# Optimization experiments

Hardware: AMD Instinct MI355X
Metric: run time of the kernel (lower is better)

## Reference

```python
import jax, jax.numpy as jnp
import numpy as np

B, T, L, H = 128, 256, 2, 512  # batch, seq_len, num_layers, hidden_size


def setup_inputs() -> dict:
    key = jax.random.key(0)
    k0, k1, k2, k3, k4 = jax.random.split(key, 5)
    s = 1.0 / np.sqrt(H).astype(np.float32)  # PyTorch LSTMCell init scale
    H0 = jax.random.normal(k0, (B, T, H), jnp.float32)
    # layers[l][k] for l in range(L), k in {0: depth cell, 1: time cell}
    Wih = jax.random.uniform(k1, (L, 2, 4 * H, H), jnp.float32, -s, s)
    Whh = jax.random.uniform(k2, (L, 2, 4 * H, H), jnp.float32, -s, s)
    bih = jax.random.uniform(k3, (L, 2, 4 * H), jnp.float32, -s, s)
    bhh = jax.random.uniform(k4, (L, 2, 4 * H), jnp.float32, -s, s)
    return {"H0": H0, "Wih": Wih, "Whh": Whh, "bih": bih, "bhh": bhh}


def _lstm_cell(x, h, c, wih, whh, b):
    # PyTorch LSTMCell gate order: i, f, g, o
    gates = x @ wih.T + h @ whh.T + b  # (B, 4H)
    i, f, g, o = jnp.split(gates, 4, axis=-1)
    c_new = jax.nn.sigmoid(f) * c + jax.nn.sigmoid(i) * jnp.tanh(g)
    h_new = jax.nn.sigmoid(o) * jnp.tanh(c_new)
    return h_new, c_new


def _forward(H0, Wih, Whh, bih, bhh):
    b = bih + bhh  # fuse the two bias terms

    def step(carry, h0_t):
        H1, M1 = carry  # (B, L, H) time-recurrent states
        h0 = h0_t  # (B, H) input at this timestep
        m0 = jnp.zeros_like(h0)  # M0 is all-zeros in the original when mem=None
        h1s, m1s = [], []
        for l in range(L):  # small static layer loop
            h1, m1 = H1[:, l], M1[:, l]
            h0, m0 = _lstm_cell(h1, h0, m0, Wih[l, 0], Whh[l, 0], b[l, 0])
            h1, m1 = _lstm_cell(h0, h1, m1, Wih[l, 1], Whh[l, 1], b[l, 1])
            h1s.append(h1)
            m1s.append(m1)
        return (jnp.stack(h1s, 1), jnp.stack(m1s, 1)), (h0, m0)

    zeros_LH = jnp.zeros((H0.shape[0], L, H), H0.dtype)
    (H1f, M1f), (H0_seq, M0_seq) = jax.lax.scan(
        step, (zeros_LH, zeros_LH), jnp.swapaxes(H0, 0, 1)
    )
    H0_out = jnp.swapaxes(H0_seq, 0, 1)  # (B, T, H)
    M0_out = jnp.swapaxes(M0_seq, 0, 1)  # (B, T, H)
    # batch_first=True -> no transpose of H1/M1 (stay (B, L, H))
    return H0_out, H1f, M0_out, M1f


def reference(H0, Wih, Whh, bih, bhh):
    # Matches torch return (H0, (H1, M0, M1)), flattened to a tuple of arrays.
    return _forward(H0, Wih, Whh, bih, bhh)
```

## Files before the change

### kernel.cpp

```cpp
#include <hip/hip_runtime.h>
#include <math.h>


static constexpr int Hn = 512;
static constexpr int Bn = 128;
static constexpr int Tn = 256;
static constexpr long THn = (long)Tn * Hn;
static constexpr long LBH = (long)Bn * Hn;
static constexpr int NBLK = 256;
static constexpr int NROUND = 2 * Tn + 1;

typedef __attribute__((ext_vector_type(8))) short short8;
typedef __attribute__((ext_vector_type(4))) float floatx4;

__device__ __forceinline__ unsigned short f2bf(float f) {
    unsigned u = __builtin_bit_cast(unsigned, f);
    unsigned r = u + 0x7FFFu + ((u >> 16) & 1u);
    return (unsigned short)(r >> 16);
}
__device__ __forceinline__ unsigned pk2(float a, float b) {
    return (unsigned)f2bf(a) | ((unsigned)f2bf(b) << 16);
}
__device__ __forceinline__ float sel4(float a, float b, float cc, float d, int s) {
    float r = a;
    r = (s == 1) ? b : r;
    r = (s == 2) ? cc : r;
    r = (s == 3) ? d : r;
    return r;
}
__device__ __forceinline__ float selc(floatx4 v, int s) {
    float r = v[0];
    r = (s == 1) ? v[1] : r;
    r = (s == 2) ? v[2] : r;
    r = (s == 3) ? v[3] : r;
    return r;
}

__device__ __forceinline__ void st16_sc(unsigned short* p, unsigned short v) {
    asm volatile("global_store_short %0, %1, off sc1" :: "v"(p), "v"(v) : "memory");
}
__device__ __forceinline__ void st32_sc(float* p, float v) {
    asm volatile("global_store_dword %0, %1, off sc1" :: "v"(p), "v"(v) : "memory");
}

struct Params {
    const float* H0in;
    const float* Wih; const float* Whh;
    const float* bih; const float* bhh;
    unsigned short* h0A; unsigned short* h0B;
    unsigned short* H1b;
    float* m0;
    float* outH0; float* outH1; float* outM0; float* outM1;
    unsigned* bar;
};

struct RoundDesc {
    const unsigned short* x;
    const unsigned short* hB;
    const float* hF;
    const float* cin;
    unsigned short* hOutB;
    float* coutA;
    long cAs;
    float* hOut2; long h2s;
    float* cOut2; long c2s;
};

__device__ __forceinline__ void gridBarrier(unsigned* bar, int leafIdx, unsigned r) {
    asm volatile("s_waitcnt vmcnt(0)" ::: "memory");
    __syncthreads();
    if (threadIdx.x == 0) {
        unsigned prev = __hip_atomic_fetch_add(&bar[leafIdx * 16], 1u,
                                               __ATOMIC_RELAXED, __HIP_MEMORY_SCOPE_AGENT);
        if ((prev & 31u) == 31u) {
            __hip_atomic_fetch_add(&bar[128], 1u, __ATOMIC_RELAXED, __HIP_MEMORY_SCOPE_AGENT);
        }
        const unsigned target = 8u * (r + 1u);
        while (__hip_atomic_load(&bar[128], __ATOMIC_RELAXED, __HIP_MEMORY_SCOPE_AGENT) < target) {
            __builtin_amdgcn_s_sleep(2);
        }
    }
    __syncthreads();
    if (threadIdx.x < 64) {
        asm volatile("buffer_inv sc1" ::: "memory");
        asm volatile("s_waitcnt vmcnt(0)" ::: "memory");
    }
    __syncthreads();
    asm volatile("" ::: "memory");
}

__device__ __forceinline__ void loadChunk(char* dst, const float* Wih, const float* Whh,
                                          int cell, int jt, int tid) {
    const int rw = tid >> 3;
    const int jj = rw >> 2, g = rw & 3;
    const long nrow = (long)cell * 2048 + (long)g * 512 + jt * 8 + jj;
    const float* baseI = Wih + nrow * 512;
    const float* baseH = Whh + nrow * 512;
    const int k0 = (tid & 7) * 128;
    #pragma unroll
    for (int i = 0; i < 16; ++i) {
        int k = k0 + i * 8;
        const float* src = (k < 512) ? (baseI + k) : (baseH + (k - 512));
        float4 v0 = *(const float4*)src;
        float4 v1 = *(const float4*)(src + 4);
        uint4 w = {pk2(v0.x, v0.y), pk2(v0.z, v0.w), pk2(v1.x, v1.y), pk2(v1.z, v1.w)};
        int byteOff = (k >> 5) * 2048 + rw * 64 + ((k >> 3) & 3) * 16;
        *(uint4*)(dst + byteOff) = w;
    }
}

template<int KIND>
__device__ __forceinline__ void runCell(const RoundDesc& D, const char* chunk,
                                        const float bias[2][4], int jt, int row0,
                                        int c, int q, float cst[2]) {
    const long arow = row0 + c;
    const int g = c & 3;
    const int cu = c >> 2;

    short8 afr[32];
    #pragma unroll
    for (int ks = 0; ks < 16; ++ks)
        afr[ks] = *(const short8*)(D.x + arow * 512 + ks * 32 + q * 8);
    if constexpr (KIND == 0) {
        #pragma unroll
        for (int ks = 0; ks < 16; ++ks) {
            const float* hp = D.hF + arow * THn + ks * 32 + q * 8;
            float4 v0 = *(const float4*)(hp);
            float4 v1 = *(const float4*)(hp + 4);
            uint4 w = {pk2(v0.x, v0.y), pk2(v0.z, v0.w),
                       pk2(v1.x, v1.y), pk2(v1.z, v1.w)};
            afr[16 + ks] = __builtin_bit_cast(short8, w);
        }
    } else {
        #pragma unroll
        for (int ks = 0; ks < 16; ++ks)
            afr[16 + ks] = *(const short8*)(D.hB + arow * 512 + ks * 32 + q * 8);
    }
    float cin0 = 0.f, cin1 = 0.f;
    if constexpr (KIND == 2) {
        const int row = row0 + q * 4 + g;
        cin0 = D.cin[(long)row * 512 + jt * 8 + cu];
        cin1 = D.cin[(long)row * 512 + jt * 8 + 4 + cu];
    }

    floatx4 acc0 = {0.f, 0.f, 0.f, 0.f};
    floatx4 acc1 = {0.f, 0.f, 0.f, 0.f};
    const char* base = chunk + (c * 64 + q * 16);
    #pragma unroll
    for (int ks = 0; ks < 32; ++ks) {
        short8 b0 = *(const short8*)(base + ks * 2048);
        short8 b1 = *(const short8*)(base + ks * 2048 + 1024);
        acc0 = __builtin_amdgcn_mfma_f32_16x16x32_bf16(afr[ks], b0, acc0, 0, 0, 0);
        acc1 = __builtin_amdgcn_mfma_f32_16x16x32_bf16(afr[ks], b1, acc1, 0, 0, 0);
    }

    #pragma unroll
    for (int nf = 0; nf < 2; ++nf) {
        floatx4 acc = nf ? acc1 : acc0;
        float s0 = selc(acc, g);
        float s1 = __shfl_xor(selc(acc, g ^ 1), 1);
        float s2 = __shfl_xor(selc(acc, g ^ 2), 2);
        float s3 = __shfl_xor(selc(acc, g ^ 3), 3);
        float iv = sel4(s0, s1, s2, s3, g)     + bias[nf][0];
        float fv = sel4(s0, s1, s2, s3, g ^ 1) + bias[nf][1];
        float gv = sel4(s0, s1, s2, s3, g ^ 2) + bias[nf][2];
        float ov = sel4(s0, s1, s2, s3, g ^ 3) + bias[nf][3];

        const int row = row0 + q * 4 + g;
        const int jglob = jt * 8 + nf * 4 + cu;
        float cold;
        if constexpr (KIND == 0)      cold = 0.f;
        else if constexpr (KIND == 2) cold = nf ? cin1 : cin0;
        else                          cold = cst[nf];
        float si = 1.f / (1.f + expf(-iv));
        float sf = 1.f / (1.f + expf(-fv));
        float so = 1.f / (1.f + expf(-ov));
        float cn = sf * cold + si * tanhf(gv);
        float hn = so * tanhf(cn);

        st16_sc(D.hOutB + (long)row * 512 + jglob, f2bf(hn));
        if constexpr (KIND == 0 || KIND == 2) {
            st32_sc(D.coutA + (long)row * D.cAs + jglob, cn);
        }
        if constexpr (KIND == 2) {
            st32_sc(D.hOut2 + (long)row * THn + jglob, hn);
        }
        if constexpr (KIND == 1 || KIND == 3) {
            cst[nf] = cn;
            if (D.hOut2) {
                st32_sc(D.hOut2 + (long)row * 1024 + jglob, hn);
                st32_sc(D.cOut2 + (long)row * 1024 + jglob, cn);
            }
        }
    }
}

__global__ __launch_bounds__(256, 1) void grid_lstm_persist(Params P) {
    __shared__ char smem[2 * 65536];

    const int tid = threadIdx.x;
    const int lane = tid & 63;
    const int wid = tid >> 6;
    const int c = lane & 15;
    const int q = lane >> 4;
    const int blk = blockIdx.x;
    const int pair = blk >> 1;
    const int half = blk & 1;
    const int jt = pair & 63;
    const bool hiPair = pair >= 64;
    const int cellA = hiPair ? 3 : 0;
    const int cellB = hiPair ? 2 : 1;
    const int leafIdx = blk & 7;

    loadChunk(smem,         P.Wih, P.Whh, cellA, jt, tid);
    loadChunk(smem + 65536, P.Wih, P.Whh, cellB, jt, tid);

    float biasA[2][4], biasB[2][4];
    {
        const int cuu = c >> 2;
        #pragma unroll
        for (int nf = 0; nf < 2; ++nf) {
            int j = jt * 8 + nf * 4 + cuu;
            #pragma unroll
            for (int g2 = 0; g2 < 4; ++g2) {
                long ia = (long)cellA * 2048 + (long)g2 * 512 + j;
                long ib = (long)cellB * 2048 + (long)g2 * 512 + j;
                biasA[nf][g2] = P.bih[ia] + P.bhh[ia];
                biasB[nf][g2] = P.bih[ib] + P.bhh[ib];
            }
        }
    }
    __syncthreads();

    const int row0 = half * 64 + wid * 16;
    float cst[2] = {0.f, 0.f};
    float cstDummy[2] = {0.f, 0.f};

    for (int r = 0; r < NROUND; ++r) {
        const int t = r >> 1;
        const bool stB = (r & 1) != 0;

        if (!stB) {
            if (!hiPair) {
                if (t < Tn) {
                    int p = t & 1;
                    RoundDesc D{};
                    D.x = P.H1b + ((long)p * 2 + 0) * LBH;
                    D.hF = P.H0in + (long)t * Hn;
                    D.hOutB = P.h0A;
                    D.coutA = P.m0; D.cAs = 512;
                    runCell<0>(D, smem, biasA, jt, row0, c, q, cstDummy);
                }
            } else {
                int tc = t - 1;
                if (tc >= 0) {
                    int p = tc & 1;
                    RoundDesc D{};
                    D.x = P.h0B;
                    D.hB = P.H1b + ((long)p * 2 + 1) * LBH;
                    D.hOutB = P.H1b + ((long)(1 - p) * 2 + 1) * LBH;
                    if (tc == Tn - 1) {
                        D.hOut2 = P.outH1 + Hn;
                        D.cOut2 = P.outM1 + Hn;
                    }
                    runCell<3>(D, smem, biasA, jt, row0, c, q, cst);
                }
            }
        } else {
            int p = t & 1;
            if (!hiPair) {
                RoundDesc D{};
                D.x = P.h0A;
                D.hB = P.H1b + ((long)p * 2 + 0) * LBH;
                D.hOutB = P.H1b + ((long)(1 - p) * 2 + 0) * LBH;
                if (t == Tn - 1) {
                    D.hOut2 = P.outH1;
                    D.cOut2 = P.outM1;
                }
                runCell<1>(D, smem + 65536, biasB, jt, row0, c, q, cst);
            } else {
                RoundDesc D{};
                D.x = P.H1b + ((long)p * 2 + 1) * LBH;
                D.hB = P.h0A;
                D.cin = P.m0;
                D.hOutB = P.h0B;
                D.coutA = P.outM0 + (long)t * Hn; D.cAs = THn;
                D.hOut2 = P.outH0 + (long)t * Hn;
                runCell<2>(D, smem + 65536, biasB, jt, row0, c, q, cstDummy);
            }
        }
        if (r + 1 < NROUND) gridBarrier(P.bar, leafIdx, (unsigned)r);
    }
}

extern "C" void kernel_launch(void* const* d_in, const int* in_sizes, int n_in,
                              void* d_out, int out_size, void* d_ws, size_t ws_size,
                              hipStream_t stream) {
    (void)in_sizes; (void)n_in; (void)out_size; (void)ws_size;
    const float* H0in = (const float*)d_in[0];
    const float* Wih  = (const float*)d_in[1];
    const float* Whh  = (const float*)d_in[2];
    const float* bih  = (const float*)d_in[3];
    const float* bhh  = (const float*)d_in[4];
    float* out = (float*)d_out;

    unsigned short* h0A = (unsigned short*)d_ws;
    unsigned short* h0B = h0A + LBH;
    unsigned short* H1b = h0B + LBH;
    float* m0 = (float*)(H1b + 4 * LBH);
    unsigned* bar = (unsigned*)(m0 + LBH);

    size_t zeroBytes = (size_t)((char*)(bar + 256) - (char*)d_ws);
    hipMemsetAsync(d_ws, 0, zeroBytes, stream);

    Params P;
    P.H0in = H0in; P.Wih = Wih; P.Whh = Whh; P.bih = bih; P.bhh = bhh;
    P.h0A = h0A; P.h0B = h0B; P.H1b = H1b; P.m0 = m0;
    P.outH0 = out;
    P.outH1 = out + (long)Bn * THn;
    P.outM0 = P.outH1 + 2 * LBH;
    P.outM1 = P.outM0 + (long)Bn * THn;
    P.bar = bar;

    void* args[] = {&P};
    hipLaunchCooperativeKernel((void*)grid_lstm_persist, dim3(NBLK), dim3(256),
                               args, 0, stream);
}
```

Measured before the change: 5.653 ms.

## Double waves per block, prefetch recurrent operands before barrier, pre-convert input to bf16

Each block now runs 512 threads, with waves split across row groups and column groups, so each wave computes one 16x16 output tile and accumulates over a 32-step K loop instead of two. The recurrent-state fragments for the next round are loaded before the grid barrier, so that load latency overlaps the barrier wait. The fp32 input sequence is converted to bf16 one timestep ahead into a double-buffered workspace, which removes the in-round fp32 loads and packing. Barrier sleep is shortened and raw s_barrier replaces __syncthreads. The cost is more registers per wave and an extra barrier round at startup.

```diff
diff --git a/kernel.cpp b/kernel.cpp
--- a/kernel.cpp
+++ b/kernel.cpp
@@ -49,6 +49,7 @@
     const float* bih; const float* bhh;
     unsigned short* h0A; unsigned short* h0B;
     unsigned short* H1b;
+    unsigned short* h0inB;
     float* m0;
     float* outH0; float* outH1; float* outM0; float* outM1;
     unsigned* bar;
@@ -57,48 +58,46 @@
 struct RoundDesc {
     const unsigned short* x;
     const unsigned short* hB;
-    const float* hF;
     const float* cin;
     unsigned short* hOutB;
     float* coutA;
-    long cAs;
-    float* hOut2; long h2s;
-    float* cOut2; long c2s;
+    float* hOut2;
+    float* cOut2;
 };
 
-__device__ __forceinline__ void gridBarrier(unsigned* bar, int leafIdx, unsigned r) {
-    asm volatile("s_waitcnt vmcnt(0)" ::: "memory");
-    __syncthreads();
+__device__ __forceinline__ void gridBarrierRaw(unsigned* bar, int leafIdx, unsigned target) {
+    __builtin_amdgcn_s_barrier();
+    asm volatile("" ::: "memory");
     if (threadIdx.x == 0) {
         unsigned prev = __hip_atomic_fetch_add(&bar[leafIdx * 16], 1u,
                                                __ATOMIC_RELAXED, __HIP_MEMORY_SCOPE_AGENT);
         if ((prev & 31u) == 31u) {
             __hip_atomic_fetch_add(&bar[128], 1u, __ATOMIC_RELAXED, __HIP_MEMORY_SCOPE_AGENT);
         }
-        const unsigned target = 8u * (r + 1u);
         while (__hip_atomic_load(&bar[128], __ATOMIC_RELAXED, __HIP_MEMORY_SCOPE_AGENT) < target) {
-            __builtin_amdgcn_s_sleep(2);
-        }
-    }
-    __syncthreads();
+            __builtin_amdgcn_s_sleep(1);
+        }
+    }
+    __builtin_amdgcn_s_barrier();
+    asm volatile("" ::: "memory");
     if (threadIdx.x < 64) {
         asm volatile("buffer_inv sc1" ::: "memory");
         asm volatile("s_waitcnt vmcnt(0)" ::: "memory");
     }
-    __syncthreads();
+    __builtin_amdgcn_s_barrier();
     asm volatile("" ::: "memory");
 }
 
 __device__ __forceinline__ void loadChunk(char* dst, const float* Wih, const float* Whh,
                                           int cell, int jt, int tid) {
-    const int rw = tid >> 3;
+    const int rw = tid >> 4;
     const int jj = rw >> 2, g = rw & 3;
     const long nrow = (long)cell * 2048 + (long)g * 512 + jt * 8 + jj;
     const float* baseI = Wih + nrow * 512;
     const float* baseH = Whh + nrow * 512;
-    const int k0 = (tid & 7) * 128;
-    #pragma unroll
-    for (int i = 0; i < 16; ++i) {
+    const int k0 = (tid & 15) * 64;
+    #pragma unroll
+    for (int i = 0; i < 8; ++i) {
         int k = k0 + i * 8;
         const float* src = (k < 512) ? (baseI + k) : (baseH + (k - 512));
         float4 v0 = *(const float4*)src;
@@ -109,93 +108,76 @@
     }
 }
 
-template<int KIND>
+template<int KIND, bool PF>
 __device__ __forceinline__ void runCell(const RoundDesc& D, const char* chunk,
-                                        const float bias[2][4], int jt, int row0,
-                                        int c, int q, float cst[2]) {
-    const long arow = row0 + c;
-    const int g = c & 3;
-    const int cu = c >> 2;
-
-    short8 afr[32];
+                                        const float bias[4], long arow, int outRow,
+                                        int jglob, int c, int q, int cg,
+                                        float& cst, const short8 pfr[16]) {
+    short8 xfr[16];
     #pragma unroll
     for (int ks = 0; ks < 16; ++ks)
-        afr[ks] = *(const short8*)(D.x + arow * 512 + ks * 32 + q * 8);
-    if constexpr (KIND == 0) {
-        #pragma unroll
-        for (int ks = 0; ks < 16; ++ks) {
-            const float* hp = D.hF + arow * THn + ks * 32 + q * 8;
-            float4 v0 = *(const float4*)(hp);
-            float4 v1 = *(const float4*)(hp + 4);
-            uint4 w = {pk2(v0.x, v0.y), pk2(v0.z, v0.w),
-                       pk2(v1.x, v1.y), pk2(v1.z, v1.w)};
-            afr[16 + ks] = __builtin_bit_cast(short8, w);
-        }
-    } else {
+        xfr[ks] = *(const short8*)(D.x + arow * 512 + ks * 32 + q * 8);
+    short8 hfr[16];
+    if constexpr (!PF) {
         #pragma unroll
         for (int ks = 0; ks < 16; ++ks)
-            afr[16 + ks] = *(const short8*)(D.hB + arow * 512 + ks * 32 + q * 8);
-    }
-    float cin0 = 0.f, cin1 = 0.f;
+            hfr[ks] = *(const short8*)(D.hB + arow * 512 + ks * 32 + q * 8);
+    }
+    float cin = 0.f;
+    if constexpr (KIND == 2)
+        cin = D.cin[(long)outRow * 512 + jglob];
+
+    floatx4 acc = {0.f, 0.f, 0.f, 0.f};
+    const char* base = chunk + ((cg * 16 + c) * 64 + q * 16);
+    #pragma unroll
+    for (int ks = 0; ks < 16; ++ks) {
+        short8 b = *(const short8*)(base + ks * 2048);
+        acc = __builtin_amdgcn_mfma_f32_16x16x32_bf16(xfr[ks], b, acc, 0, 0, 0);
+    }
+    #pragma unroll
+    for (int ks = 0; ks < 16; ++ks) {
+        short8 b = *(const short8*)(base + (16 + ks) * 2048);
+        const short8 a = PF ? pfr[ks] : hfr[ks];
+        acc = __builtin_amdgcn_mfma_f32_16x16x32_bf16(a, b, acc, 0, 0, 0);
+    }
+
+    const int g = c & 3;
+    float s0 = selc(acc, g);
+    float s1 = __shfl_xor(selc(acc, g ^ 1), 1);
+    float s2 = __shfl_xor(selc(acc, g ^ 2), 2);
+    float s3 = __shfl_xor(selc(acc, g ^ 3), 3);
+    float iv = sel4(s0, s1, s2, s3, g)     + bias[0];
+    float fv = sel4(s0, s1, s2, s3, g ^ 1) + bias[1];
+    float gv = sel4(s0, s1, s2, s3, g ^ 2) + bias[2];
+    float ov = sel4(s0, s1, s2, s3, g ^ 3) + bias[3];
+
+    float cold;
+    if constexpr (KIND == 0)      cold = 0.f;
+    else if constexpr (KIND == 2) cold = cin;
+    else                          cold = cst;
+    float si = 1.f / (1.f + expf(-iv));
+    float sf = 1.f / (1.f + expf(-fv));
+    float so = 1.f / (1.f + expf(-ov));
+    float cn = sf * cold + si * tanhf(gv);
+    float hn = so * tanhf(cn);
+
+    st16_sc(D.hOutB + (long)outRow * 512 + jglob, f2bf(hn));
+    if constexpr (KIND == 0)
+        st32_sc(D.coutA + (long)outRow * 512 + jglob, cn);
     if constexpr (KIND == 2) {
-        const int row = row0 + q * 4 + g;
-        cin0 = D.cin[(long)row * 512 + jt * 8 + cu];
-        cin1 = D.cin[(long)row * 512 + jt * 8 + 4 + cu];
-    }
-
-    floatx4 acc0 = {0.f, 0.f, 0.f, 0.f};
-    floatx4 acc1 = {0.f, 0.f, 0.f, 0.f};
-    const char* base = chunk + (c * 64 + q * 16);
-    #pragma unroll
-    for (int ks = 0; ks < 32; ++ks) {
-        short8 b0 = *(const short8*)(base + ks * 2048);
-        short8 b1 = *(const short8*)(base + ks * 2048 + 1024);
-        acc0 = __builtin_amdgcn_mfma_f32_16x16x32_bf16(afr[ks], b0, acc0, 0, 0, 0);
-        acc1 = __builtin_amdgcn_mfma_f32_16x16x32_bf16(afr[ks], b1, acc1, 0, 0, 0);
-    }
-
-    #pragma unroll
-    for (int nf = 0; nf < 2; ++nf) {
-        floatx4 acc = nf ? acc1 : acc0;
-        float s0 = selc(acc, g);
-        float s1 = __shfl_xor(selc(acc, g ^ 1), 1);
-        float s2 = __shfl_xor(selc(acc, g ^ 2), 2);
-        float s3 = __shfl_xor(selc(acc, g ^ 3), 3);
-        float iv = sel4(s0, s1, s2, s3, g)     + bias[nf][0];
-        float fv = sel4(s0, s1, s2, s3, g ^ 1) + bias[nf][1];
-        float gv = sel4(s0, s1, s2, s3, g ^ 2) + bias[nf][2];
-        float ov = sel4(s0, s1, s2, s3, g ^ 3) + bias[nf][3];
-
-        const int row = row0 + q * 4 + g;
-        const int jglob = jt * 8 + nf * 4 + cu;
-        float cold;
-        if constexpr (KIND == 0)      cold = 0.f;
-        else if constexpr (KIND == 2) cold = nf ? cin1 : cin0;
-        else                          cold = cst[nf];
-        float si = 1.f / (1.f + expf(-iv));
-        float sf = 1.f / (1.f + expf(-fv));
-        float so = 1.f / (1.f + expf(-ov));
-        float cn = sf * cold + si * tanhf(gv);
-        float hn = so * tanhf(cn);
-
-        st16_sc(D.hOutB + (long)row * 512 + jglob, f2bf(hn));
-        if constexpr (KIND == 0 || KIND == 2) {
-            st32_sc(D.coutA + (long)row * D.cAs + jglob, cn);
-        }
-        if constexpr (KIND == 2) {
-            st32_sc(D.hOut2 + (long)row * THn + jglob, hn);
-        }
-        if constexpr (KIND == 1 || KIND == 3) {
-            cst[nf] = cn;
-            if (D.hOut2) {
-                st32_sc(D.hOut2 + (long)row * 1024 + jglob, hn);
-                st32_sc(D.cOut2 + (long)row * 1024 + jglob, cn);
-            }
-        }
-    }
-}
-
-__global__ __launch_bounds__(256, 1) void grid_lstm_persist(Params P) {
+        st32_sc(D.coutA + (long)outRow * THn + jglob, cn);
+        st32_sc(D.hOut2 + (long)outRow * THn + jglob, hn);
+    }
+    if constexpr (KIND == 1 || KIND == 3) {
+        cst = cn;
+        if (D.hOut2) {
+            st32_sc(D.hOut2 + (long)outRow * 1024 + jglob, hn);
+            st32_sc(D.cOut2 + (long)outRow * 1024 + jglob, cn);
+        }
+    }
+}
+
+__global__ __launch_bounds__(512, 2) void grid_lstm_persist(Params P) {
     __shared__ char smem[2 * 65536];
 
     const int tid = threadIdx.x;
@@ -203,6 +185,8 @@
     const int wid = tid >> 6;
     const int c = lane & 15;
     const int q = lane >> 4;
+    const int rg = wid & 3;
+    const int cg = wid >> 2;
     const int blk = blockIdx.x;
     const int pair = blk >> 1;
     const int half = blk & 1;
@@ -215,30 +199,43 @@
     loadChunk(smem,         P.Wih, P.Whh, cellA, jt, tid);
     loadChunk(smem + 65536, P.Wih, P.Whh, cellB, jt, tid);
 
-    float biasA[2][4], biasB[2][4];
-    {
-        const int cuu = c >> 2;
-        #pragma unroll
-        for (int nf = 0; nf < 2; ++nf) {
-            int j = jt * 8 + nf * 4 + cuu;
-            #pragma unroll
-            for (int g2 = 0; g2 < 4; ++g2) {
-                long ia = (long)cellA * 2048 + (long)g2 * 512 + j;
-                long ib = (long)cellB * 2048 + (long)g2 * 512 + j;
-                biasA[nf][g2] = P.bih[ia] + P.bhh[ia];
-                biasB[nf][g2] = P.bih[ib] + P.bhh[ib];
-            }
-        }
+    const int row0 = half * 64 + rg * 16;
+    const long arow = row0 + c;
+    const int jglob = jt * 8 + cg * 4 + (c >> 2);
+    const int outRow = row0 + q * 4 + (c & 3);
+
+    float biasA[4], biasB[4];
+    #pragma unroll
+    for (int g2 = 0; g2 < 4; ++g2) {
+        long ia = (long)cellA * 2048 + (long)g2 * 512 + jglob;
+        long ib = (long)cellB * 2048 + (long)g2 * 512 + jglob;
+        biasA[g2] = P.bih[ia] + P.bhh[ia];
+        biasB[g2] = P.bih[ib] + P.bhh[ib];
+    }
+
+    if (tid < 256) {
+        int idx = blk * 256 + tid;
+        float hv = P.H0in[(long)(idx >> 9) * THn + (idx & 511)];
+        st16_sc(P.h0inB + idx, f2bf(hv));
     }
     __syncthreads();
-
-    const int row0 = half * 64 + wid * 16;
-    float cst[2] = {0.f, 0.f};
-    float cstDummy[2] = {0.f, 0.f};
+    asm volatile("s_waitcnt vmcnt(0)" ::: "memory");
+    unsigned bnum = 1;
+    gridBarrierRaw(P.bar, leafIdx, 8u * bnum); ++bnum;
+
+    float cst = 0.f;
+    short8 pfr[16];
 
     for (int r = 0; r < NROUND; ++r) {
         const int t = r >> 1;
         const bool stB = (r & 1) != 0;
+
+        const bool doConv = (!stB) && (t + 1 < Tn) && (tid < 256);
+        float convV = 0.f; int convIdx = 0;
+        if (doConv) {
+            convIdx = blk * 256 + tid;
+            convV = P.H0in[(long)(convIdx >> 9) * THn + (long)(t + 1) * Hn + (convIdx & 511)];
+        }
 
         if (!stB) {
             if (!hiPair) {
@@ -246,10 +243,11 @@
                     int p = t & 1;
                     RoundDesc D{};
                     D.x = P.H1b + ((long)p * 2 + 0) * LBH;
-                    D.hF = P.H0in + (long)t * Hn;
+                    D.hB = P.h0inB + (long)(t & 1) * LBH;
                     D.hOutB = P.h0A;
-                    D.coutA = P.m0; D.cAs = 512;
-                    runCell<0>(D, smem, biasA, jt, row0, c, q, cstDummy);
+                    D.coutA = P.m0;
+                    if (r == 0) runCell<0, false>(D, smem, biasA, arow, outRow, jglob, c, q, cg, cst, pfr);
+                    else        runCell<0, true >(D, smem, biasA, arow, outRow, jglob, c, q, cg, cst, pfr);
                 }
             } else {
                 int tc = t - 1;
@@ -257,13 +255,12 @@
                     int p = tc & 1;
                     RoundDesc D{};
                     D.x = P.h0B;
-                    D.hB = P.H1b + ((long)p * 2 + 1) * LBH;
                     D.hOutB = P.H1b + ((long)(1 - p) * 2 + 1) * LBH;
                     if (tc == Tn - 1) {
                         D.hOut2 = P.outH1 + Hn;
                         D.cOut2 = P.outM1 + Hn;
                     }
-                    runCell<3>(D, smem, biasA, jt, row0, c, q, cst);
+                    runCell<3, true>(D, smem, biasA, arow, outRow, jglob, c, q, cg, cst, pfr);
                 }
             }
         } else {
@@ -271,25 +268,49 @@
             if (!hiPair) {
                 RoundDesc D{};
                 D.x = P.h0A;
-                D.hB = P.H1b + ((long)p * 2 + 0) * LBH;
                 D.hOutB = P.H1b + ((long)(1 - p) * 2 + 0) * LBH;
                 if (t == Tn - 1) {
                     D.hOut2 = P.outH1;
                     D.cOut2 = P.outM1;
                 }
-                runCell<1>(D, smem + 65536, biasB, jt, row0, c, q, cst);
+                runCell<1, true>(D, smem + 65536, biasB, arow, outRow, jglob, c, q, cg, cst, pfr);
             } else {
                 RoundDesc D{};
                 D.x = P.H1b + ((long)p * 2 + 1) * LBH;
                 D.hB = P.h0A;
                 D.cin = P.m0;
                 D.hOutB = P.h0B;
-                D.coutA = P.outM0 + (long)t * Hn; D.cAs = THn;
+                D.coutA = P.outM0 + (long)t * Hn;
                 D.hOut2 = P.outH0 + (long)t * Hn;
-                runCell<2>(D, smem + 65536, biasB, jt, row0, c, q, cstDummy);
+                runCell<2, false>(D, smem + 65536, biasB, arow, outRow, jglob, c, q, cg, cst, pfr);
             }
         }
-        if (r + 1 < NROUND) gridBarrier(P.bar, leafIdx, (unsigned)r);
+
+        if (doConv)
+            st16_sc(P.h0inB + (long)((t + 1) & 1) * LBH + convIdx, f2bf(convV));
+
+        if (r + 1 < NROUND) {
+            asm volatile("s_waitcnt vmcnt(0)" ::: "memory");
+            const unsigned short* hp = nullptr;
+            if (!hiPair) {
+                if (((r + 1) & 1) != 0) {
+                    hp = P.H1b + ((long)(t & 1) * 2 + 0) * LBH;
+                } else if (t + 1 < Tn) {
+                    hp = P.h0inB + (long)((t + 1) & 1) * LBH;
+                }
+            } else {
+                if (((r + 1) & 1) == 0) {
+                    int tcn = ((r + 1) >> 1) - 1;
+                    hp = P.H1b + ((long)(tcn & 1) * 2 + 1) * LBH;
+                }
+            }
+            if (hp) {
+                #pragma unroll
+                for (int ks = 0; ks < 16; ++ks)
+                    pfr[ks] = *(const short8*)(hp + arow * 512 + ks * 32 + q * 8);
+            }
+            gridBarrierRaw(P.bar, leafIdx, 8u * bnum); ++bnum;
+        }
     }
 }
 
@@ -309,13 +330,14 @@
     unsigned short* H1b = h0B + LBH;
     float* m0 = (float*)(H1b + 4 * LBH);
     unsigned* bar = (unsigned*)(m0 + LBH);
+    unsigned short* h0inB = (unsigned short*)(bar + 256);
 
     size_t zeroBytes = (size_t)((char*)(bar + 256) - (char*)d_ws);
     hipMemsetAsync(d_ws, 0, zeroBytes, stream);
 
     Params P;
     P.H0in = H0in; P.Wih = Wih; P.Whh = Whh; P.bih = bih; P.bhh = bhh;
-    P.h0A = h0A; P.h0B = h0B; P.H1b = H1b; P.m0 = m0;
+    P.h0A = h0A; P.h0B = h0B; P.H1b = H1b; P.h0inB = h0inB; P.m0 = m0;
     P.outH0 = out;
     P.outH1 = out + (long)Bn * THn;
     P.outM0 = P.outH1 + 2 * LBH;
@@ -323,6 +345,6 @@
     P.bar = bar;
 
     void* args[] = {&P};
-    hipLaunchCooperativeKernel((void*)grid_lstm_persist, dim3(NBLK), dim3(256),
+    hipLaunchCooperativeKernel((void*)grid_lstm_persist, dim3(NBLK), dim3(512),
                                args, 0, stream);
 }
```

After: 7.259 ms. +28.4%, slower.
